# Performance work log

Hardware: AMD Instinct MI355X
Metric: run time of the kernel (lower is better)

The kernel has to match this reference:

```python
import jax, jax.numpy as jnp
import numpy as np

N_NODES = 100000
N_EDGES = 1600000
BN_EPS = 1e-5
NUM_LAYER = 20


def setup_inputs() -> dict:
    key = jax.random.key(0)
    ks = jax.random.split(key, 10)
    inp = {
        "M": jax.random.normal(ks[0], (N_NODES, 3), dtype=jnp.float32),
        "H": jax.random.normal(ks[1], (N_EDGES, 3), dtype=jnp.float32),
        "edge_index": jax.random.randint(ks[2], (2, N_EDGES), 0, N_NODES, dtype=jnp.int32),
        # mlp_e: Linear(9,4) -> BN(4) -> ReLU -> Linear(4,3)
        "we_w1": jax.random.normal(ks[3], (9, 4), dtype=jnp.float32) * 0.3,
        "we_b1": jnp.zeros((4,), jnp.float32),
        "we_g1": jnp.ones((4,), jnp.float32),
        "we_be1": jnp.zeros((4,), jnp.float32),
        "we_w2": jax.random.normal(ks[4], (4, 3), dtype=jnp.float32) * 0.3,
        "we_b2": jnp.zeros((3,), jnp.float32),
        # mlp_v: Linear(6,3) -> BN(3) -> ReLU -> Linear(3,3)
        "wv_w1": jax.random.normal(ks[5], (6, 3), dtype=jnp.float32) * 0.3,
        "wv_b1": jnp.zeros((3,), jnp.float32),
        "wv_g1": jnp.ones((3,), jnp.float32),
        "wv_be1": jnp.zeros((3,), jnp.float32),
        "wv_w2": jax.random.normal(ks[6], (3, 3), dtype=jnp.float32) * 0.3,
        "wv_b2": jnp.zeros((3,), jnp.float32),
        # head: Linear(3,3) -> BN(3) -> ReLU -> Linear(3,2) -> Softmax
        "out_w1": jax.random.normal(ks[7], (3, 3), dtype=jnp.float32) * 0.3,
        "out_b1": jnp.zeros((3,), jnp.float32),
        "out_g": jnp.ones((3,), jnp.float32),
        "out_be": jnp.zeros((3,), jnp.float32),
        "out_w2": jax.random.normal(ks[8], (3, 2), dtype=jnp.float32) * 0.3,
        "out_b2": jnp.zeros((2,), jnp.float32),
    }
    return inp


def _bn(x, g, b):
    # BatchNorm1d in training mode: batch stats, biased variance
    m = jnp.mean(x, axis=0)
    v = jnp.mean(jnp.square(x - m), axis=0)
    return (x - m) * jax.lax.rsqrt(v + BN_EPS) * g + b


def reference(M, H, edge_index, we_w1, we_b1, we_g1, we_be1, we_w2, we_b2,
              wv_w1, wv_b1, wv_g1, wv_be1, wv_w2, wv_b2,
              out_w1, out_b1, out_g, out_be, out_w2, out_b2):
    src = edge_index[0]  # _j (source, flow=source_to_target)
    dst = edge_index[1]  # _i (target), also the aggregation index
    n = M.shape[0]

    def layer(carry, _):
        M, H = carry
        Mi = M[dst]  # [E,3] gather of target node feats
        Mj = M[src]  # [E,3] gather of source node feats
        e_in = jnp.concatenate([Mi, Mj, H], axis=1)  # [E,9]
        Hn = jax.nn.relu(_bn(e_in @ we_w1 + we_b1, we_g1, we_be1)) @ we_w2 + we_b2  # [E,3]
        v_in = jnp.concatenate([Mi, Hn], axis=1)  # [E,6]
        Mmsg = jax.nn.relu(_bn(v_in @ wv_w1 + wv_b1, wv_g1, wv_be1)) @ wv_w2 + wv_b2  # [E,3]
        Mn = jax.ops.segment_sum(Mmsg, dst, num_segments=n)  # scatter-add to targets
        return (Mn, Hn), None

    (M, H), _ = jax.lax.scan(layer, (M, H), None, length=NUM_LAYER)
    logits = jax.nn.relu(_bn(H @ out_w1 + out_b1, out_g, out_be)) @ out_w2 + out_b2  # [E,2]
    return jax.nn.softmax(logits, axis=1)
```

## Files before the change

kernel.cpp:

```cpp
#include <hip/hip_runtime.h>
#include <hip/hip_fp16.h>
#include <math.h>

#define NNODES 100000
#define NEDGES 1600000
#define NGROUP (NEDGES / 4)
#define NLAYERS 20
#define NB 256
#define BLK 256
#define GRIDE 1024
#define STRIDE (GRIDE * BLK)
#define GRIDL ((NGROUP + BLK - 1) / BLK)
#define NBLKN ((NNODES + 255) / 256)

struct __align__(8) H4 { __half h[4]; };

template<int N>
__device__ __forceinline__ void block_stats_atomic(const float* vals, double* base) {
  __shared__ double sm[16][4];
  int lane = threadIdx.x & 63, wid = threadIdx.x >> 6;
  __syncthreads();
  #pragma unroll
  for (int n = 0; n < N; ++n) {
    double d = (double)vals[n];
    #pragma unroll
    for (int o = 32; o > 0; o >>= 1) d += __shfl_down(d, o, 64);
    if (lane == 0) sm[n][wid] = d;
  }
  __syncthreads();
  if (threadIdx.x < N) {
    double s = sm[threadIdx.x][0] + sm[threadIdx.x][1] + sm[threadIdx.x][2] + sm[threadIdx.x][3];
    atomicAdd(base + threadIdx.x, s);
  }
}

template<int NS>
__device__ __forceinline__ void bank_reduce(const double* __restrict__ acc, double* res) {
  __shared__ double red[BLK * 8];
  int t = threadIdx.x;
  #pragma unroll
  for (int s = 0; s < NS; ++s) red[t * 8 + s] = acc[t * 8 + s];
  __syncthreads();
  for (int o = BLK / 2; o > 0; o >>= 1) {
    if (t < o) {
      #pragma unroll
      for (int s = 0; s < NS; ++s) red[t * 8 + s] += red[(t + o) * 8 + s];
    }
    __syncthreads();
  }
  #pragma unroll
  for (int s = 0; s < NS; ++s) res[s] = red[s];
  __syncthreads();
}

__device__ __forceinline__ void compute_x(const float4 mi, const float4 mj,
    float h0, float h1, float h2,
    const float* __restrict__ w, const float* __restrict__ b, float* x) {
  #pragma unroll
  for (int j = 0; j < 4; ++j) {
    float t = b[j];
    t += mi.x * w[0 * 4 + j]; t += mi.y * w[1 * 4 + j]; t += mi.z * w[2 * 4 + j];
    t += mj.x * w[3 * 4 + j]; t += mj.y * w[4 * 4 + j]; t += mj.z * w[5 * 4 + j];
    t += h0 * w[6 * 4 + j];  t += h1 * w[7 * 4 + j];  t += h2 * w[8 * 4 + j];
    x[j] = t;
  }
}

__global__ void __launch_bounds__(BLK) kz(const float* __restrict__ Min,
                                          float* __restrict__ M,
                                          int* __restrict__ hist,
                                          double* __restrict__ accs) {
  int tid = blockIdx.x * BLK + threadIdx.x;
  for (int v = tid; v < NNODES; v += STRIDE) {
    float4 m;
    m.x = Min[3 * v]; m.y = Min[3 * v + 1]; m.z = Min[3 * v + 2]; m.w = 0.f;
    *(float4*)(M + 4 * (size_t)v) = m;
    hist[v] = 0;
  }
  for (int i = tid; i < 3 * NB * 8; i += STRIDE) accs[i] = 0.0;
}

__global__ void __launch_bounds__(BLK) khr(const int* __restrict__ dst,
                                           int* __restrict__ hist,
                                           int* __restrict__ rankpos) {
  int g = blockIdx.x * BLK + threadIdx.x;
  if (g >= NGROUP) return;
  int4 d4 = ((const int4*)dst)[g];
  int4 r;
  r.x = atomicAdd(&hist[d4.x], 1);
  r.y = atomicAdd(&hist[d4.y], 1);
  r.z = atomicAdd(&hist[d4.z], 1);
  r.w = atomicAdd(&hist[d4.w], 1);
  ((int4*)rankpos)[g] = r;
}

__global__ void __launch_bounds__(256) ksA(const int* __restrict__ hist,
                                           int* __restrict__ bsum) {
  __shared__ int sm[256];
  int i = blockIdx.x * 256 + threadIdx.x;
  sm[threadIdx.x] = (i < NNODES) ? hist[i] : 0;
  __syncthreads();
  for (int o = 128; o > 0; o >>= 1) {
    if (threadIdx.x < o) sm[threadIdx.x] += sm[threadIdx.x + o];
    __syncthreads();
  }
  if (threadIdx.x == 0) bsum[blockIdx.x] = sm[0];
}

__global__ void __launch_bounds__(512) ksB(const int* __restrict__ bsum,
                                           int* __restrict__ bbase) {
  __shared__ int sm[512];
  int t = threadIdx.x;
  sm[t] = (t < NBLKN) ? bsum[t] : 0;
  __syncthreads();
  for (int o = 1; o < 512; o <<= 1) {
    int v = (t >= o) ? sm[t - o] : 0;
    __syncthreads();
    sm[t] += v;
    __syncthreads();
  }
  if (t < NBLKN) bbase[t] = (t == 0) ? 0 : sm[t - 1];
}

__global__ void __launch_bounds__(256) ksC(const int* __restrict__ hist,
                                           const int* __restrict__ bbase,
                                           int* __restrict__ off) {
  __shared__ int sm[256];
  int t = threadIdx.x;
  int i = blockIdx.x * 256 + t;
  int v = (i < NNODES) ? hist[i] : 0;
  sm[t] = v;
  __syncthreads();
  for (int o = 1; o < 256; o <<= 1) {
    int u = (t >= o) ? sm[t - o] : 0;
    __syncthreads();
    sm[t] += u;
    __syncthreads();
  }
  if (i < NNODES) off[i] = bbase[blockIdx.x] + sm[t] - v;
  if (i == 0) off[NNODES] = NEDGES;
}

__global__ void __launch_bounds__(BLK) kp1(const int* __restrict__ dst,
                                           const int* __restrict__ off,
                                           int* __restrict__ rankpos,
                                           int* __restrict__ eperm) {
  int g = blockIdx.x * BLK + threadIdx.x;
  if (g >= NGROUP) return;
  int4 d4 = ((const int4*)dst)[g];
  int4 r4 = ((int4*)rankpos)[g];
  int4 p4;
  p4.x = off[d4.x] + r4.x;
  p4.y = off[d4.y] + r4.y;
  p4.z = off[d4.z] + r4.z;
  p4.w = off[d4.w] + r4.w;
  int e = 4 * g;
  eperm[p4.x] = e; eperm[p4.y] = e + 1; eperm[p4.z] = e + 2; eperm[p4.w] = e + 3;
  ((int4*)rankpos)[g] = p4;
}

__global__ void __launch_bounds__(BLK) kp2(const int* __restrict__ src,
                                           const int* __restrict__ dst,
                                           const float* __restrict__ Hin,
                                           const int* __restrict__ eperm,
                                           int* __restrict__ sp,
                                           int* __restrict__ dp,
                                           __half* __restrict__ Hp) {
  int g = blockIdx.x * BLK + threadIdx.x;
  if (g >= NGROUP) return;
  int4 e4 = ((const int4*)eperm)[g];
  int4 s4, d4;
  s4.x = src[e4.x]; d4.x = dst[e4.x];
  s4.y = src[e4.y]; d4.y = dst[e4.y];
  s4.z = src[e4.z]; d4.z = dst[e4.z];
  s4.w = src[e4.w]; d4.w = dst[e4.w];
  __half hh[12];
  int ee[4] = {e4.x, e4.y, e4.z, e4.w};
  #pragma unroll
  for (int k = 0; k < 4; ++k) {
    size_t e3 = 3 * (size_t)ee[k];
    hh[3 * k]     = __float2half(Hin[e3]);
    hh[3 * k + 1] = __float2half(Hin[e3 + 1]);
    hh[3 * k + 2] = __float2half(Hin[e3 + 2]);
  }
  ((int4*)sp)[g] = s4;
  ((int4*)dp)[g] = d4;
  H4* Hv = (H4*)(Hp + 12 * (size_t)g);
  H4 a, b, c;
  #pragma unroll
  for (int i = 0; i < 4; ++i) { a.h[i] = hh[i]; b.h[i] = hh[4 + i]; c.h[i] = hh[8 + i]; }
  Hv[0] = a; Hv[1] = b; Hv[2] = c;
}

__global__ void __launch_bounds__(BLK) k1(
    const float* __restrict__ M, const __half* __restrict__ H,
    const int* __restrict__ sp, const int* __restrict__ dp,
    const float* __restrict__ W1, const float* __restrict__ b1,
    double* __restrict__ acc1, double* __restrict__ acc2) {
  int g = blockIdx.x * BLK + threadIdx.x;
  if (blockIdx.x == 0)
    for (int i = threadIdx.x; i < NB * 8; i += BLK) acc2[i] = 0.0;

  float sx[4] = {0, 0, 0, 0}, sq[4] = {0, 0, 0, 0};
  if (g < NGROUP) {
    int4 s4 = ((const int4*)sp)[g];
    int4 d4 = ((const int4*)dp)[g];
    const H4* Hv = (const H4*)(H + 12 * (size_t)g);
    H4 a = Hv[0], b = Hv[1], c = Hv[2];
    float hf[12];
    #pragma unroll
    for (int i = 0; i < 4; ++i) {
      hf[i] = __half2float(a.h[i]); hf[4 + i] = __half2float(b.h[i]); hf[8 + i] = __half2float(c.h[i]);
    }
    float4 mi0 = *(const float4*)(M + 4 * (size_t)d4.x);
    float4 mj0 = *(const float4*)(M + 4 * (size_t)s4.x);
    float4 mi1 = *(const float4*)(M + 4 * (size_t)d4.y);
    float4 mj1 = *(const float4*)(M + 4 * (size_t)s4.y);
    float4 mi2 = *(const float4*)(M + 4 * (size_t)d4.z);
    float4 mj2 = *(const float4*)(M + 4 * (size_t)s4.z);
    float4 mi3 = *(const float4*)(M + 4 * (size_t)d4.w);
    float4 mj3 = *(const float4*)(M + 4 * (size_t)s4.w);
    float x[4][4];
    compute_x(mi0, mj0, hf[0], hf[1], hf[2],  W1, b1, x[0]);
    compute_x(mi1, mj1, hf[3], hf[4], hf[5],  W1, b1, x[1]);
    compute_x(mi2, mj2, hf[6], hf[7], hf[8],  W1, b1, x[2]);
    compute_x(mi3, mj3, hf[9], hf[10], hf[11], W1, b1, x[3]);
    #pragma unroll
    for (int k = 0; k < 4; ++k)
      #pragma unroll
      for (int j = 0; j < 4; ++j) { sx[j] += x[k][j]; sq[j] += x[k][j] * x[k][j]; }
  }
  float vals[8] = {sx[0], sx[1], sx[2], sx[3], sq[0], sq[1], sq[2], sq[3]};
  block_stats_atomic<8>(vals, acc1 + (size_t)(blockIdx.x & (NB - 1)) * 8);
}

__global__ void __launch_bounds__(BLK) k2(
    const float* __restrict__ M, const __half* __restrict__ H, __half* __restrict__ Hn,
    const int* __restrict__ sp, const int* __restrict__ dp,
    const float* __restrict__ W1, const float* __restrict__ b1,
    const float* __restrict__ g1, const float* __restrict__ be1,
    const float* __restrict__ W2, const float* __restrict__ b2,
    const float* __restrict__ V1, const float* __restrict__ vb1,
    const double* __restrict__ acc1, double* __restrict__ acc2,
    int isFinal,
    const float* __restrict__ OW1, const float* __restrict__ ob1,
    double* __restrict__ accF) {
  double red[8];
  bank_reduce<8>(acc1, red);
  float s1[4], t1[4];
  {
    const double invE = 1.0 / (double)NEDGES;
    #pragma unroll
    for (int j = 0; j < 4; ++j) {
      double m = red[j] * invE;
      double var = red[4 + j] * invE - m * m;
      double sc = (double)g1[j] / sqrt(var + 1e-5);
      s1[j] = (float)sc;
      t1[j] = (float)((double)be1[j] - m * sc);
    }
  }
  float sz[3] = {0, 0, 0}, szz[3] = {0, 0, 0}, sf[3] = {0, 0, 0}, sff[3] = {0, 0, 0};
  int g = blockIdx.x * BLK + threadIdx.x;
  if (g < NGROUP) {
    int4 s4 = ((const int4*)sp)[g];
    int4 d4 = ((const int4*)dp)[g];
    const H4* Hv = (const H4*)(H + 12 * (size_t)g);
    H4 ha = Hv[0], hb = Hv[1], hc = Hv[2];
    float hf[12];
    #pragma unroll
    for (int i = 0; i < 4; ++i) {
      hf[i] = __half2float(ha.h[i]); hf[4 + i] = __half2float(hb.h[i]); hf[8 + i] = __half2float(hc.h[i]);
    }
    float4 mi[4], mj[4];
    mi[0] = *(const float4*)(M + 4 * (size_t)d4.x);
    mj[0] = *(const float4*)(M + 4 * (size_t)s4.x);
    mi[1] = *(const float4*)(M + 4 * (size_t)d4.y);
    mj[1] = *(const float4*)(M + 4 * (size_t)s4.y);
    mi[2] = *(const float4*)(M + 4 * (size_t)d4.z);
    mj[2] = *(const float4*)(M + 4 * (size_t)s4.z);
    mi[3] = *(const float4*)(M + 4 * (size_t)d4.w);
    mj[3] = *(const float4*)(M + 4 * (size_t)s4.w);
    __half hh[12];
    float hnr[4][3];
    #pragma unroll
    for (int k = 0; k < 4; ++k) {
      float x[4], y[4];
      compute_x(mi[k], mj[k], hf[3 * k], hf[3 * k + 1], hf[3 * k + 2], W1, b1, x);
      #pragma unroll
      for (int j = 0; j < 4; ++j) y[j] = fmaxf(x[j] * s1[j] + t1[j], 0.f);
      #pragma unroll
      for (int c = 0; c < 3; ++c) {
        float v = b2[c] + y[0] * W2[0 * 3 + c] + y[1] * W2[1 * 3 + c]
                        + y[2] * W2[2 * 3 + c] + y[3] * W2[3 * 3 + c];
        __half hv = __float2half(v);
        hh[3 * k + c] = hv;
        hnr[k][c] = __half2float(hv);
      }
      #pragma unroll
      for (int c = 0; c < 3; ++c) {
        float z = vb1[c] + mi[k].x * V1[0 * 3 + c] + mi[k].y * V1[1 * 3 + c] + mi[k].z * V1[2 * 3 + c]
                         + hnr[k][0] * V1[3 * 3 + c] + hnr[k][1] * V1[4 * 3 + c] + hnr[k][2] * V1[5 * 3 + c];
        sz[c] += z; szz[c] += z * z;
      }
      if (isFinal) {
        #pragma unroll
        for (int c = 0; c < 3; ++c) {
          float f = ob1[c] + hnr[k][0] * OW1[0 * 3 + c] + hnr[k][1] * OW1[1 * 3 + c] + hnr[k][2] * OW1[2 * 3 + c];
          sf[c] += f; sff[c] += f * f;
        }
      }
    }
    H4* Hw = (H4*)(Hn + 12 * (size_t)g);
    H4 oA, oB, oC;
    #pragma unroll
    for (int i = 0; i < 4; ++i) { oA.h[i] = hh[i]; oB.h[i] = hh[4 + i]; oC.h[i] = hh[8 + i]; }
    Hw[0] = oA; Hw[1] = oB; Hw[2] = oC;
  }
  size_t bank = (size_t)(blockIdx.x & (NB - 1)) * 8;
  float v6[6] = {sz[0], sz[1], sz[2], szz[0], szz[1], szz[2]};
  block_stats_atomic<6>(v6, acc2 + bank);
  if (isFinal) {
    float v6b[6] = {sf[0], sf[1], sf[2], sff[0], sff[1], sff[2]};
    block_stats_atomic<6>(v6b, accF + bank);
  }
}

__global__ void __launch_bounds__(BLK) k3(
    const float* __restrict__ M, const __half* __restrict__ Hn,
    const int* __restrict__ off,
    const float* __restrict__ V1, const float* __restrict__ vb1,
    const float* __restrict__ vg1, const float* __restrict__ vbe1,
    const float* __restrict__ V2, const float* __restrict__ vb2,
    const double* __restrict__ acc2, double* __restrict__ acc1,
    float* __restrict__ Mnew) {
  double red[6];
  bank_reduce<6>(acc2, red);
  float s2[3], t2[3];
  {
    const double invE = 1.0 / (double)NEDGES;
    #pragma unroll
    for (int c = 0; c < 3; ++c) {
      double m = red[c] * invE;
      double var = red[3 + c] * invE - m * m;
      double sc = (double)vg1[c] / sqrt(var + 1e-5);
      s2[c] = (float)sc;
      t2[c] = (float)((double)vbe1[c] - m * sc);
    }
  }
  if (blockIdx.x == 0)
    for (int i = threadIdx.x; i < NB * 8; i += BLK) acc1[i] = 0.0;

  int v = blockIdx.x * BLK + threadIdx.x;
  if (v >= NNODES) return;
  float4 mi = *(const float4*)(M + 4 * (size_t)v);
  int e0 = off[v], e1 = off[v + 1];
  float a0 = 0.f, a1 = 0.f, a2v = 0.f;
  for (int e = e0; e < e1; ++e) {
    size_t e3 = 3 * (size_t)e;
    float h0 = __half2float(Hn[e3]), h1 = __half2float(Hn[e3 + 1]), h2 = __half2float(Hn[e3 + 2]);
    float y[3];
    #pragma unroll
    for (int c = 0; c < 3; ++c) {
      float z = vb1[c] + mi.x * V1[0 * 3 + c] + mi.y * V1[1 * 3 + c] + mi.z * V1[2 * 3 + c]
                       + h0 * V1[3 * 3 + c] + h1 * V1[4 * 3 + c] + h2 * V1[5 * 3 + c];
      y[c] = fmaxf(z * s2[c] + t2[c], 0.f);
    }
    a0  += vb2[0] + y[0] * V2[0] + y[1] * V2[3] + y[2] * V2[6];
    a1  += vb2[1] + y[0] * V2[1] + y[1] * V2[4] + y[2] * V2[7];
    a2v += vb2[2] + y[0] * V2[2] + y[1] * V2[5] + y[2] * V2[8];
  }
  float4 o; o.x = a0; o.y = a1; o.z = a2v; o.w = 0.f;
  *(float4*)(Mnew + 4 * (size_t)v) = o;
}

__global__ void __launch_bounds__(BLK) f2(
    const __half* __restrict__ H, const int* __restrict__ pos,
    const float* __restrict__ OW1, const float* __restrict__ ob1,
    const float* __restrict__ og, const float* __restrict__ obe,
    const float* __restrict__ OW2, const float* __restrict__ ob2,
    const double* __restrict__ accF, float* __restrict__ out) {
  double red[6];
  bank_reduce<6>(accF, red);
  float sF[3], tF[3];
  {
    const double invE = 1.0 / (double)NEDGES;
    #pragma unroll
    for (int c = 0; c < 3; ++c) {
      double m = red[c] * invE;
      double var = red[3 + c] * invE - m * m;
      double sc = (double)og[c] / sqrt(var + 1e-5);
      sF[c] = (float)sc;
      tF[c] = (float)((double)obe[c] - m * sc);
    }
  }
  int g = blockIdx.x * BLK + threadIdx.x;
  if (g >= NGROUP) return;
  int4 p4 = ((const int4*)pos)[g];
  int p[4] = {p4.x, p4.y, p4.z, p4.w};
  float2 o[4];
  #pragma unroll
  for (int k = 0; k < 4; ++k) {
    size_t p3 = 3 * (size_t)p[k];
    float h0 = __half2float(H[p3]), h1 = __half2float(H[p3 + 1]), h2 = __half2float(H[p3 + 2]);
    float y[3];
    #pragma unroll
    for (int c = 0; c < 3; ++c) {
      float f = ob1[c] + h0 * OW1[0 * 3 + c] + h1 * OW1[1 * 3 + c] + h2 * OW1[2 * 3 + c];
      y[c] = fmaxf(f * sF[c] + tF[c], 0.f);
    }
    float l0 = ob2[0] + y[0] * OW2[0] + y[1] * OW2[2] + y[2] * OW2[4];
    float l1 = ob2[1] + y[0] * OW2[1] + y[1] * OW2[3] + y[2] * OW2[5];
    float mx = fmaxf(l0, l1);
    float e0 = __expf(l0 - mx), e1 = __expf(l1 - mx);
    float inv = 1.f / (e0 + e1);
    o[k].x = e0 * inv; o[k].y = e1 * inv;
  }
  float4 oA, oB;
  oA.x = o[0].x; oA.y = o[0].y; oA.z = o[1].x; oA.w = o[1].y;
  oB.x = o[2].x; oB.y = o[2].y; oB.z = o[3].x; oB.w = o[3].y;
  ((float4*)out)[2 * (size_t)g] = oA;
  ((float4*)out)[2 * (size_t)g + 1] = oB;
}

extern "C" void kernel_launch(void* const* d_in, const int* in_sizes, int n_in,
                              void* d_out, int out_size, void* d_ws, size_t ws_size,
                              hipStream_t stream) {
  const float* M_in   = (const float*)d_in[0];
  const float* H_in   = (const float*)d_in[1];
  const int*   ei     = (const int*)d_in[2];
  const float* we_w1  = (const float*)d_in[3];
  const float* we_b1  = (const float*)d_in[4];
  const float* we_g1  = (const float*)d_in[5];
  const float* we_be1 = (const float*)d_in[6];
  const float* we_w2  = (const float*)d_in[7];
  const float* we_b2  = (const float*)d_in[8];
  const float* wv_w1  = (const float*)d_in[9];
  const float* wv_b1  = (const float*)d_in[10];
  const float* wv_g1  = (const float*)d_in[11];
  const float* wv_be1 = (const float*)d_in[12];
  const float* wv_w2  = (const float*)d_in[13];
  const float* wv_b2  = (const float*)d_in[14];
  const float* out_w1 = (const float*)d_in[15];
  const float* out_b1 = (const float*)d_in[16];
  const float* out_g  = (const float*)d_in[17];
  const float* out_be = (const float*)d_in[18];
  const float* out_w2 = (const float*)d_in[19];
  const float* out_b2 = (const float*)d_in[20];
  const int* src = ei;
  const int* dst = ei + NEDGES;

  float* ws = (float*)d_ws;
  float* MA  = ws;
  float* MB  = ws + 400000;
  __half* Hp0 = (__half*)(ws + 800000);
  __half* Hp1 = (__half*)(ws + 3200000);
  int* eperm  = (int*)Hp1;
  int* ib      = (int*)(ws + 5600000);
  int* sp      = ib;
  int* dp      = ib + 1600000;
  int* rankpos = ib + 3200000;
  int* hist    = ib + 4800000;
  int* off     = ib + 4900000;
  int* bsum    = ib + 5000001;
  int* bbase   = ib + 5000401;
  double* accs = (double*)(ws + 5600000 + 5000802);
  double* acc1 = accs;
  double* acc2 = accs + NB * 8;
  double* accF = accs + 2 * NB * 8;

  kz<<<GRIDE, BLK, 0, stream>>>(M_in, MA, hist, accs);
  khr<<<GRIDL, BLK, 0, stream>>>(dst, hist, rankpos);
  ksA<<<NBLKN, 256, 0, stream>>>(hist, bsum);
  ksB<<<1, 512, 0, stream>>>(bsum, bbase);
  ksC<<<NBLKN, 256, 0, stream>>>(hist, bbase, off);
  kp1<<<GRIDL, BLK, 0, stream>>>(dst, off, rankpos, eperm);
  kp2<<<GRIDL, BLK, 0, stream>>>(src, dst, H_in, eperm, sp, dp, Hp0);

  for (int l = 0; l < NLAYERS; ++l) {
    const float* Mc = (l & 1) ? MB : MA;
    float*       Mn = (l & 1) ? MA : MB;
    const __half* Hc = (l & 1) ? Hp1 : Hp0;
    __half*       Hw = (l & 1) ? Hp0 : Hp1;
    k1<<<GRIDL, BLK, 0, stream>>>(Mc, Hc, sp, dp, we_w1, we_b1, acc1, acc2);
    k2<<<GRIDL, BLK, 0, stream>>>(Mc, Hc, Hw, sp, dp, we_w1, we_b1, we_g1, we_be1,
                                  we_w2, we_b2, wv_w1, wv_b1, acc1, acc2,
                                  (l == NLAYERS - 1) ? 1 : 0, out_w1, out_b1, accF);
    if (l < NLAYERS - 1)
      k3<<<NBLKN, BLK, 0, stream>>>(
          Mc, Hw, off, wv_w1, wv_b1, wv_g1, wv_be1, wv_w2, wv_b2, acc2, acc1, Mn);
  }
  f2<<<GRIDL, BLK, 0, stream>>>(Hp0, rankpos, out_w1, out_b1, out_g, out_be,
                                out_w2, out_b2, accF, (float*)d_out);
}
```

Baseline: 1.277 ms.

## Split per-node aggregation across four lanes and build sorted dst from CSR offsets

The per-node segment-sum kernel now gives each node four threads. Each thread strides over the node's CSR edges, and the partial sums are combined with width-4 shuffles. This raises parallelism and lets neighbouring lanes read adjacent edges. The sorted dst array is now filled directly from the CSR offsets in a new kernel instead of gathered through the permutation in kp2, which removes a random gather. There are more threads with idle lanes for low-degree nodes, plus one extra setup launch.

Result: faster. 1.224 ms (-4.2%).

```diff
diff --git a/kernel.cpp b/kernel.cpp
--- a/kernel.cpp
+++ b/kernel.cpp
@@ -12,6 +12,7 @@
 #define STRIDE (GRIDE * BLK)
 #define GRIDL ((NGROUP + BLK - 1) / BLK)
 #define NBLKN ((NNODES + 255) / 256)
+#define GRIDN4 ((NNODES * 4 + BLK - 1) / BLK)
 
 struct __align__(8) H4 { __half h[4]; };
 
@@ -139,6 +140,14 @@
   }
   if (i < NNODES) off[i] = bbase[blockIdx.x] + sm[t] - v;
   if (i == 0) off[NNODES] = NEDGES;
+}
+
+__global__ void __launch_bounds__(BLK) kd(const int* __restrict__ off,
+                                          int* __restrict__ dp) {
+  int v = blockIdx.x * BLK + threadIdx.x;
+  if (v >= NNODES) return;
+  int e0 = off[v], e1 = off[v + 1];
+  for (int e = e0; e < e1; ++e) dp[e] = v;
 }
 
 __global__ void __launch_bounds__(BLK) kp1(const int* __restrict__ dst,
@@ -160,20 +169,18 @@
 }
 
 __global__ void __launch_bounds__(BLK) kp2(const int* __restrict__ src,
-                                           const int* __restrict__ dst,
                                            const float* __restrict__ Hin,
                                            const int* __restrict__ eperm,
                                            int* __restrict__ sp,
-                                           int* __restrict__ dp,
                                            __half* __restrict__ Hp) {
   int g = blockIdx.x * BLK + threadIdx.x;
   if (g >= NGROUP) return;
   int4 e4 = ((const int4*)eperm)[g];
-  int4 s4, d4;
-  s4.x = src[e4.x]; d4.x = dst[e4.x];
-  s4.y = src[e4.y]; d4.y = dst[e4.y];
-  s4.z = src[e4.z]; d4.z = dst[e4.z];
-  s4.w = src[e4.w]; d4.w = dst[e4.w];
+  int4 s4;
+  s4.x = src[e4.x];
+  s4.y = src[e4.y];
+  s4.z = src[e4.z];
+  s4.w = src[e4.w];
   __half hh[12];
   int ee[4] = {e4.x, e4.y, e4.z, e4.w};
   #pragma unroll
@@ -184,7 +191,6 @@
     hh[3 * k + 2] = __float2half(Hin[e3 + 2]);
   }
   ((int4*)sp)[g] = s4;
-  ((int4*)dp)[g] = d4;
   H4* Hv = (H4*)(Hp + 12 * (size_t)g);
   H4 a, b, c;
   #pragma unroll
@@ -350,12 +356,13 @@
   if (blockIdx.x == 0)
     for (int i = threadIdx.x; i < NB * 8; i += BLK) acc1[i] = 0.0;
 
-  int v = blockIdx.x * BLK + threadIdx.x;
+  int idx = blockIdx.x * BLK + threadIdx.x;
+  int v = idx >> 2, q = idx & 3;
   if (v >= NNODES) return;
   float4 mi = *(const float4*)(M + 4 * (size_t)v);
   int e0 = off[v], e1 = off[v + 1];
   float a0 = 0.f, a1 = 0.f, a2v = 0.f;
-  for (int e = e0; e < e1; ++e) {
+  for (int e = e0 + q; e < e1; e += 4) {
     size_t e3 = 3 * (size_t)e;
     float h0 = __half2float(Hn[e3]), h1 = __half2float(Hn[e3 + 1]), h2 = __half2float(Hn[e3 + 2]);
     float y[3];
@@ -369,8 +376,13 @@
     a1  += vb2[1] + y[0] * V2[1] + y[1] * V2[4] + y[2] * V2[7];
     a2v += vb2[2] + y[0] * V2[2] + y[1] * V2[5] + y[2] * V2[8];
   }
-  float4 o; o.x = a0; o.y = a1; o.z = a2v; o.w = 0.f;
-  *(float4*)(Mnew + 4 * (size_t)v) = o;
+  a0  += __shfl_down(a0, 2, 4);  a0  += __shfl_down(a0, 1, 4);
+  a1  += __shfl_down(a1, 2, 4);  a1  += __shfl_down(a1, 1, 4);
+  a2v += __shfl_down(a2v, 2, 4); a2v += __shfl_down(a2v, 1, 4);
+  if (q == 0) {
+    float4 o; o.x = a0; o.y = a1; o.z = a2v; o.w = 0.f;
+    *(float4*)(Mnew + 4 * (size_t)v) = o;
+  }
 }
 
 __global__ void __launch_bounds__(BLK) f2(
@@ -473,8 +485,9 @@
   ksA<<<NBLKN, 256, 0, stream>>>(hist, bsum);
   ksB<<<1, 512, 0, stream>>>(bsum, bbase);
   ksC<<<NBLKN, 256, 0, stream>>>(hist, bbase, off);
+  kd<<<NBLKN, BLK, 0, stream>>>(off, dp);
   kp1<<<GRIDL, BLK, 0, stream>>>(dst, off, rankpos, eperm);
-  kp2<<<GRIDL, BLK, 0, stream>>>(src, dst, H_in, eperm, sp, dp, Hp0);
+  kp2<<<GRIDL, BLK, 0, stream>>>(src, H_in, eperm, sp, Hp0);
 
   for (int l = 0; l < NLAYERS; ++l) {
     const float* Mc = (l & 1) ? MB : MA;
@@ -486,7 +499,7 @@
                                   we_w2, we_b2, wv_w1, wv_b1, acc1, acc2,
                                   (l == NLAYERS - 1) ? 1 : 0, out_w1, out_b1, accF);
     if (l < NLAYERS - 1)
-      k3<<<NBLKN, BLK, 0, stream>>>(
+      k3<<<GRIDN4, BLK, 0, stream>>>(
           Mc, Hw, off, wv_w1, wv_b1, wv_g1, wv_be1, wv_w2, wv_b2, acc2, acc1, Mn);
   }
   f2<<<GRIDL, BLK, 0, stream>>>(Hp0, rankpos, out_w1, out_b1, out_g, out_be,
```
